# Performance work log

Measured on AMD Instinct MI355X. Metric: run time of the kernel, lower is better.

Reference implementation:

```python
import jax, jax.numpy as jnp
import numpy as np

REPEAT_STEP = 4  # speculative_num_draft_tokens


def setup_inputs() -> dict:
    key = jax.random.key(0)
    k1, k2, k3, k4, k5 = jax.random.split(key, 5)
    BS = 512
    M = BS * REPEAT_STEP          # 2048 expanded rows
    LEN_A = 16384
    LEN_B = 128
    LEN_OUT = LEN_A + LEN_B
    return {
        "page_table_dst": jax.random.randint(k1, (M, LEN_OUT), 0, 1000000, dtype=jnp.int32),
        "page_table_a": jax.random.randint(k2, (BS, LEN_A), 0, 1000000, dtype=jnp.int32),
        "page_table_b": jax.random.randint(k3, (M, LEN_B), 0, 1000000, dtype=jnp.int32),
        "seq_len_a": jax.random.randint(k4, (BS,), 0, LEN_A, dtype=jnp.int32),
        "seq_len_b": jax.random.randint(k5, (M,), 0, LEN_B, dtype=jnp.int32),
    }


def reference(page_table_dst, page_table_a, page_table_b, seq_len_a, seq_len_b):
    M, LEN_OUT = page_table_dst.shape
    LEN_A = page_table_a.shape[1]
    LEN_B = page_table_b.shape[1]

    idx_a = jnp.arange(M) // REPEAT_STEP            # [M] map expanded row -> base row
    sa = seq_len_a[idx_a][:, None]                  # [M,1]
    sb = seq_len_b[:, None]                         # [M,1]
    offs = jnp.arange(LEN_OUT)[None, :]             # [1,LEN_OUT]

    # source-A values: gather the base row, valid where offs < seq_len_a (and in bounds)
    a_rows = page_table_a[idx_a]                    # [M, LEN_A]
    a_idx = jnp.broadcast_to(jnp.clip(offs, 0, LEN_A - 1), (M, LEN_OUT))
    a_val = jnp.take_along_axis(a_rows, a_idx, axis=1)
    a_val = jnp.where((offs < sa) & (offs < LEN_A), a_val, 0)

    # source-B values: shifted by seq_len_a per row
    b_offs = offs - sa                              # [M,LEN_OUT]
    b_idx = jnp.clip(b_offs, 0, LEN_B - 1)
    b_val = jnp.take_along_axis(page_table_b, b_idx, axis=1)
    b_val = jnp.where((b_offs >= 0) & (b_offs < sb) & (b_offs < LEN_B), b_val, 0)

    spliced = jnp.where(offs < sa, a_val, b_val)
    total = sa + sb
    # positions beyond total_len keep the original dst contents (kernel masks stores)
    return jnp.where(offs < total, spliced, page_table_dst)
```

## Files before the change

kernel.cpp:

```cpp
#include <hip/hip_runtime.h>


typedef int v4i __attribute__((ext_vector_type(4)));

__device__ __forceinline__ v4i splice_vec(
    int vc, int sa, int total, int nA, int nTail,
    const int* __restrict__ a_row, const int* __restrict__ b_row,
    const int* __restrict__ dst_row)
{
    const int j0 = vc << 2;
    if (vc < nA) {
        return *(const v4i*)(a_row + j0);
    } else if (vc >= nTail) {
        return __builtin_nontemporal_load((const v4i*)(dst_row + j0));
    } else {
        v4i v;
#pragma unroll
        for (int t = 0; t < 4; ++t) {
            const int j = j0 + t;
            v[t] = (j < sa) ? a_row[j] : ((j < total) ? b_row[j - sa] : dst_row[j]);
        }
        return v;
    }
}

__global__ __launch_bounds__(256) void splice_kernel(
    const int* __restrict__ dst,
    const int* __restrict__ a,
    const int* __restrict__ b,
    const int* __restrict__ seq_a,
    const int* __restrict__ seq_b,
    int* __restrict__ out,
    int LEN_OUT, int LEN_A, int LEN_B, int repeat_shift)
{
    const int m   = blockIdx.x;
    const int tid = threadIdx.x;

    const int ia    = m >> repeat_shift;
    const int sa    = seq_a[ia];
    const int sb    = seq_b[m];
    const int total = sa + sb;
    const int nvec  = LEN_OUT >> 2;
    const int nA    = sa >> 2;
    const int nTail = (total + 3) >> 2;

    const int* a_row   = a   + (size_t)ia * LEN_A;
    const int* b_row   = b   + (size_t)m  * LEN_B;
    const int* dst_row = dst + (size_t)m  * LEN_OUT;
    int*       out_row = out + (size_t)m  * LEN_OUT;

    const int full = nvec >> 8;
#pragma unroll 4
    for (int k = 0; k < full; ++k) {
        const int vc = (k << 8) + tid;
        v4i v = splice_vec(vc, sa, total, nA, nTail, a_row, b_row, dst_row);
        __builtin_nontemporal_store(v, (v4i*)(out_row + (vc << 2)));
    }
    const int vc = (full << 8) + tid;
    if (vc < nvec) {
        v4i v = splice_vec(vc, sa, total, nA, nTail, a_row, b_row, dst_row);
        __builtin_nontemporal_store(v, (v4i*)(out_row + (vc << 2)));
    }
}

extern "C" void kernel_launch(void* const* d_in, const int* in_sizes, int n_in,
                              void* d_out, int out_size, void* d_ws, size_t ws_size,
                              hipStream_t stream) {
    const int* dst   = (const int*)d_in[0];
    const int* a     = (const int*)d_in[1];
    const int* b     = (const int*)d_in[2];
    const int* seq_a = (const int*)d_in[3];
    const int* seq_b = (const int*)d_in[4];
    int* out = (int*)d_out;

    const int BS      = in_sizes[3];
    const int M       = in_sizes[4];
    const int LEN_A   = in_sizes[1] / BS;
    const int LEN_B   = in_sizes[2] / M;
    const int LEN_OUT = in_sizes[0] / M;
    const int repeat  = M / BS;
    int repeat_shift = 0;
    while ((1 << repeat_shift) < repeat) ++repeat_shift;

    splice_kernel<<<dim3(M), dim3(256), 0, stream>>>(dst, a, b, seq_a, seq_b, out,
                                                     LEN_OUT, LEN_A, LEN_B, repeat_shift);
}
```

Before: 252.2 us.

## Process four draft rows per block, loading each page_table_a vector once

```diff
diff --git a/kernel.cpp b/kernel.cpp
--- a/kernel.cpp
+++ b/kernel.cpp
@@ -3,63 +3,62 @@
 
 typedef int v4i __attribute__((ext_vector_type(4)));
 
-__device__ __forceinline__ v4i splice_vec(
-    int vc, int sa, int total, int nA, int nTail,
-    const int* __restrict__ a_row, const int* __restrict__ b_row,
-    const int* __restrict__ dst_row)
-{
-    const int j0 = vc << 2;
-    if (vc < nA) {
-        return *(const v4i*)(a_row + j0);
-    } else if (vc >= nTail) {
-        return __builtin_nontemporal_load((const v4i*)(dst_row + j0));
-    } else {
-        v4i v;
-#pragma unroll
-        for (int t = 0; t < 4; ++t) {
-            const int j = j0 + t;
-            v[t] = (j < sa) ? a_row[j] : ((j < total) ? b_row[j - sa] : dst_row[j]);
-        }
-        return v;
-    }
-}
-
-__global__ __launch_bounds__(256) void splice_kernel(
+__global__ __launch_bounds__(1024) void splice4_kernel(
     const int* __restrict__ dst,
     const int* __restrict__ a,
     const int* __restrict__ b,
     const int* __restrict__ seq_a,
     const int* __restrict__ seq_b,
     int* __restrict__ out,
-    int LEN_OUT, int LEN_A, int LEN_B, int repeat_shift)
+    int LEN_OUT, int LEN_A, int LEN_B)
 {
-    const int m   = blockIdx.x;
+    const int ia  = blockIdx.x;
     const int tid = threadIdx.x;
+    const int m0  = ia << 2;
 
-    const int ia    = m >> repeat_shift;
-    const int sa    = seq_a[ia];
-    const int sb    = seq_b[m];
-    const int total = sa + sb;
-    const int nvec  = LEN_OUT >> 2;
-    const int nA    = sa >> 2;
-    const int nTail = (total + 3) >> 2;
+    const int sa   = seq_a[ia];
+    const int nA   = sa >> 2;
+    const int nvec = LEN_OUT >> 2;
 
-    const int* a_row   = a   + (size_t)ia * LEN_A;
-    const int* b_row   = b   + (size_t)m  * LEN_B;
-    const int* dst_row = dst + (size_t)m  * LEN_OUT;
-    int*       out_row = out + (size_t)m  * LEN_OUT;
+    int sb[4], total[4], nTail[4];
+    const int *b_row[4], *dst_row[4];
+    int *out_row[4];
+#pragma unroll
+    for (int r = 0; r < 4; ++r) {
+        const int m = m0 + r;
+        sb[r]    = seq_b[m];
+        total[r] = sa + sb[r];
+        nTail[r] = (total[r] + 3) >> 2;
+        b_row[r]   = b   + (size_t)m * LEN_B;
+        dst_row[r] = dst + (size_t)m * LEN_OUT;
+        out_row[r] = out + (size_t)m * LEN_OUT;
+    }
+    const int* a_row = a + (size_t)ia * LEN_A;
 
-    const int full = nvec >> 8;
-#pragma unroll 4
-    for (int k = 0; k < full; ++k) {
-        const int vc = (k << 8) + tid;
-        v4i v = splice_vec(vc, sa, total, nA, nTail, a_row, b_row, dst_row);
-        __builtin_nontemporal_store(v, (v4i*)(out_row + (vc << 2)));
-    }
-    const int vc = (full << 8) + tid;
-    if (vc < nvec) {
-        v4i v = splice_vec(vc, sa, total, nA, nTail, a_row, b_row, dst_row);
-        __builtin_nontemporal_store(v, (v4i*)(out_row + (vc << 2)));
+    for (int vc = tid; vc < nvec; vc += 1024) {
+        const int j0 = vc << 2;
+        if (vc < nA) {
+            const v4i va = *(const v4i*)(a_row + j0);
+#pragma unroll
+            for (int r = 0; r < 4; ++r)
+                __builtin_nontemporal_store(va, (v4i*)(out_row[r] + j0));
+        } else {
+#pragma unroll
+            for (int r = 0; r < 4; ++r) {
+                v4i v;
+                if (vc >= nTail[r]) {
+                    v = __builtin_nontemporal_load((const v4i*)(dst_row[r] + j0));
+                } else {
+#pragma unroll
+                    for (int t = 0; t < 4; ++t) {
+                        const int j = j0 + t;
+                        v[t] = (j < sa) ? a_row[j]
+                             : ((j < total[r]) ? b_row[r][j - sa] : dst_row[r][j]);
+                    }
+                }
+                __builtin_nontemporal_store(v, (v4i*)(out_row[r] + j0));
+            }
+        }
     }
 }
 
@@ -78,10 +77,7 @@
     const int LEN_A   = in_sizes[1] / BS;
     const int LEN_B   = in_sizes[2] / M;
     const int LEN_OUT = in_sizes[0] / M;
-    const int repeat  = M / BS;
-    int repeat_shift = 0;
-    while ((1 << repeat_shift) < repeat) ++repeat_shift;
 
-    splice_kernel<<<dim3(M), dim3(256), 0, stream>>>(dst, a, b, seq_a, seq_b, out,
-                                                     LEN_OUT, LEN_A, LEN_B, repeat_shift);
+    splice4_kernel<<<dim3(BS), dim3(1024), 0, stream>>>(dst, a, b, seq_a, seq_b, out,
+                                                        LEN_OUT, LEN_A, LEN_B);
 }
```

After: 248.8 us. About the same (-1.3%).
